# Kernel optimization log

Hardware: AMD Instinct MI355X
Metric: run time of the kernel (lower is better)

The kernel has to match this reference:

```python
import jax, jax.numpy as jnp
import numpy as np

VOCAB, EMB, HID, NCLASS = 32000, 256, 512, 16
SEQ, BATCH = 512, 128


def setup_inputs() -> dict:
    key = jax.random.key(0)
    ks = jax.random.split(key, 8)
    s = 1.0 / np.sqrt(HID)
    return {
        "x": jax.random.randint(ks[0], (SEQ, BATCH), 0, VOCAB, dtype=jnp.int32),
        "emb": jax.random.normal(ks[1], (VOCAB, EMB), dtype=jnp.float32),
        "W_ih": jax.random.uniform(ks[2], (HID, EMB), jnp.float32, -s, s),
        "W_hh": jax.random.uniform(ks[3], (HID, HID), jnp.float32, -s, s),
        "b_ih": jax.random.uniform(ks[4], (HID,), jnp.float32, -s, s),
        "b_hh": jax.random.uniform(ks[5], (HID,), jnp.float32, -s, s),
        "W_fc": jax.random.uniform(ks[6], (NCLASS, HID), jnp.float32, -s, s),
        "b_fc": jax.random.uniform(ks[7], (NCLASS,), jnp.float32, -s, s),
    }


def reference(x, emb, W_ih, W_hh, b_ih, b_hh, W_fc, b_fc):
    # embedding lookup: [S, B] -> [S, B, E]
    xe = emb[x]
    # precompute input projections for all timesteps: [S, B, H]
    xproj = jnp.einsum("sbe,he->sbh", xe, W_ih) + b_ih + b_hh

    def step(h, xp_t):
        h_new = jnp.tanh(xp_t + h @ W_hh.T)
        return h_new, None

    h0 = jnp.zeros((xe.shape[1], W_hh.shape[0]), dtype=xe.dtype)
    h_last, _ = jax.lax.scan(step, h0, xproj)
    # final linear on last timestep's hidden state: [B, NCLASS]
    return h_last @ W_fc.T + b_fc
```

## Files before the change

### kernel.cpp

```cpp
#include <hip/hip_runtime.h>
#include <hip/hip_bf16.h>

#define SEQ   512
#define BATCH 128
#define EMBD  256
#define HIDD  512
#define NCLS  16
#define VOCAB 32000

typedef unsigned long long u64;
typedef __attribute__((ext_vector_type(8))) short  short8;
typedef __attribute__((ext_vector_type(4))) float  f32x4;
typedef __attribute__((ext_vector_type(4))) int    i32x4;

__device__ __forceinline__ float bfu(unsigned short u) {
    return __uint_as_float(((unsigned int)u) << 16);
}
__device__ __forceinline__ unsigned short f2bf(float f) {
    __hip_bfloat16 h = __float2bfloat16(f);
    return *reinterpret_cast<unsigned short*>(&h);
}
__device__ __forceinline__ float rcp_fast(float x) {
    float r;
    asm("v_rcp_f32 %0, %1" : "=v"(r) : "v"(x));
    return r;
}
__device__ __forceinline__ unsigned q127b(float x) {
    const float e = __expf(x + x);
    const float r = rcp_fast(e + 1.f);
    const float f = fmaf(r, -254.f, 12583039.f);
    return __float_as_uint(f);
}
__device__ __forceinline__ unsigned pack4(unsigned a, unsigned b,
                                          unsigned c, unsigned d) {
    const unsigned lo = __builtin_amdgcn_perm(b, a, 0x0400u);
    const unsigned hi = __builtin_amdgcn_perm(d, c, 0x0400u);
    return __builtin_amdgcn_perm(hi, lo, 0x05040100u);
}
__device__ __forceinline__ void ep_store(unsigned short* p, float v) { *p = f2bf(v); }

__device__ __forceinline__ void lds_barrier() {
    __builtin_amdgcn_sched_barrier(0);
    asm volatile("s_waitcnt lgkmcnt(0)" ::: "memory");
    __builtin_amdgcn_s_barrier();
    __builtin_amdgcn_sched_barrier(0);
}

__global__ void init_scl(float* __restrict__ scl) {
    if (threadIdx.x == 0) reinterpret_cast<unsigned*>(scl)[2] = 0u;
}

__global__ __launch_bounds__(256) void absmax_whh2(const float* __restrict__ W,
                                                   float* __restrict__ scl) {
    __shared__ float red[256];
    float m = 0.f;
    for (int i = blockIdx.x * 256 + threadIdx.x; i < (HIDD * HIDD) / 4; i += 64 * 256) {
        const float4 v = reinterpret_cast<const float4*>(W)[i];
        m = fmaxf(m, fmaxf(fmaxf(fabsf(v.x), fabsf(v.y)),
                           fmaxf(fabsf(v.z), fabsf(v.w))));
    }
    red[threadIdx.x] = m;
    __syncthreads();
    for (int s = 128; s > 0; s >>= 1) {
        if (threadIdx.x < s) red[threadIdx.x] = fmaxf(red[threadIdx.x], red[threadIdx.x + s]);
        __syncthreads();
    }
    if (threadIdx.x == 0)
        atomicMax(reinterpret_cast<unsigned*>(scl) + 2, __float_as_uint(red[0]));
}

__global__ void quant_whh2(const float* __restrict__ W, float* __restrict__ scl,
                           signed char* __restrict__ Wq) {
    const int i = blockIdx.x * 256 + threadIdx.x;
    const float am  = __uint_as_float(reinterpret_cast<unsigned*>(scl)[2]);
    const float inv = 127.f / am;
    Wq[i] = (signed char)(int)rintf(W[i] * inv);
    if (i == 0) { scl[0] = am; scl[1] = am / 16129.f; }
}

__global__ void cvt_wih(const float* __restrict__ W, unsigned short* __restrict__ Wb) {
    const int i = blockIdx.x * 256 + threadIdx.x;
    Wb[i] = f2bf(W[i]);
}

__global__ __launch_bounds__(256) void ep_gemm3(
    const float* __restrict__ emb, const unsigned short* __restrict__ Wih_b,
    const float* __restrict__ b_ih, const float* __restrict__ b_hh,
    unsigned short* __restrict__ EP) {
    const int w = threadIdx.x >> 6, l = threadIdx.x & 63;
    const int n = l & 15, lk = l >> 4;
    const int mtile = blockIdx.x * 4 + w;
    const int arow  = mtile * 16 + n;

    short8 areg[8];
    #pragma unroll
    for (int kk = 0; kk < 8; ++kk) {
        const int k0 = kk * 32 + lk * 8;
        const float4 a0 = *reinterpret_cast<const float4*>(emb + arow * EMBD + k0);
        const float4 a1 = *reinterpret_cast<const float4*>(emb + arow * EMBD + k0 + 4);
        short8 t;
        t[0]=(short)f2bf(a0.x); t[1]=(short)f2bf(a0.y); t[2]=(short)f2bf(a0.z); t[3]=(short)f2bf(a0.w);
        t[4]=(short)f2bf(a1.x); t[5]=(short)f2bf(a1.y); t[6]=(short)f2bf(a1.z); t[7]=(short)f2bf(a1.w);
        areg[kk] = t;
    }

    for (int nt = 0; nt < 32; ++nt) {
        const int col  = nt * 16 + n;
        const float bias = b_ih[col] + b_hh[col];
        f32x4 accA = {0.f,0.f,0.f,0.f}, accB = {0.f,0.f,0.f,0.f};
        #pragma unroll
        for (int kk = 0; kk < 8; ++kk) {
            const short8 bb = *reinterpret_cast<const short8*>(
                Wih_b + (size_t)col * EMBD + kk * 32 + lk * 8);
            if (kk & 1) accB = __builtin_amdgcn_mfma_f32_16x16x32_bf16(areg[kk], bb, accB, 0, 0, 0);
            else        accA = __builtin_amdgcn_mfma_f32_16x16x32_bf16(areg[kk], bb, accA, 0, 0, 0);
        }
        const f32x4 ac = accA + accB;
        #pragma unroll
        for (int r = 0; r < 4; ++r)
            ep_store(EP + (size_t)(mtile * 16 + lk * 4 + r) * HIDD + col, ac[r] + bias);
    }
}

__global__ __launch_bounds__(512, 2) void rnn11(
    const int*            __restrict__ x,
    const signed char*    __restrict__ Wq,
    const float*          __restrict__ scl,
    const unsigned short* __restrict__ EP,
    const float*          __restrict__ W_fc,
    const float*          __restrict__ b_fc,
    float*                __restrict__ out) {

    __shared__ __align__(16) char hq[2 * 16 * 512];

    const int tid = threadIdx.x;
    const int w   = tid >> 6, l = tid & 63;
    const int n   = l & 15,  lk = l >> 4;
    const int b0  = blockIdx.x * 16;
    const int jw  = w * 64;
    const float fs = scl[1];

    int rdA[8];
    #pragma unroll
    for (int kf = 0; kf < 8; ++kf) {
        const int g = kf * 4 + lk;
        rdA[kf] = n * 512 + ((g ^ n) << 4);
    }
    int wrA[4];
    #pragma unroll
    for (int tau = 0; tau < 4; ++tau) {
        const int j0 = jw + tau * 16 + lk * 4;
        wrA[tau] = n * 512 + (((j0 >> 4) ^ n) << 4) + (j0 & 15);
    }

    const unsigned short* const epb = EP + jw + lk * 4;

    i32x4 af[4][8];
    #pragma unroll
    for (int tau = 0; tau < 4; ++tau)
        #pragma unroll
        for (int kf = 0; kf < 8; ++kf)
            af[tau][kf] = *reinterpret_cast<const i32x4*>(
                Wq + (size_t)(jw + tau * 16 + n) * HIDD + kf * 64 + lk * 16);

    {
        const int tok0 = x[b0 + n];
        #pragma unroll
        for (int tau = 0; tau < 4; ++tau) {
            const ushort4 v = *reinterpret_cast<const ushort4*>(
                epb + (size_t)tok0 * HIDD + tau * 16);
            *reinterpret_cast<unsigned*>(hq + 8192 + wrA[tau]) =
                pack4(q127b(bfu(v.x)), q127b(bfu(v.y)),
                      q127b(bfu(v.z)), q127b(bfu(v.w)));
        }
    }

    ushort4 pcA[4], pcB[4];
    int tokA, tokB;
    {
        const int tok1 = x[BATCH + b0 + n];
        #pragma unroll
        for (int tau = 0; tau < 4; ++tau)
            pcA[tau] = *reinterpret_cast<const ushort4*>(
                epb + (size_t)tok1 * HIDD + tau * 16);
    }
    tokB = x[2 * BATCH + b0 + n];
    __syncthreads();

#define FIN(tau, acc, PC, WO)                                                 \
    {                                                                         \
        const unsigned q0 = q127b(fmaf((float)acc[0], fs, bfu(PC[tau].x)));   \
        const unsigned q1 = q127b(fmaf((float)acc[1], fs, bfu(PC[tau].y)));   \
        const unsigned q2 = q127b(fmaf((float)acc[2], fs, bfu(PC[tau].z)));   \
        const unsigned q3 = q127b(fmaf((float)acc[3], fs, bfu(PC[tau].w)));   \
        *reinterpret_cast<unsigned*>(hq + (WO) + wrA[tau]) = pack4(q0, q1, q2, q3); \
    }
#define STEP(ro, wo, PC, PN, TOKIN, TOKOUT, TNEXT)                            \
    {                                                                         \
        _Pragma("unroll")                                                     \
        for (int tau = 0; tau < 4; ++tau)                                     \
            PN[tau] = *reinterpret_cast<const ushort4*>(                      \
                epb + (size_t)(TOKIN) * HIDD + tau * 16);                     \
        const int tn_ = (TNEXT) > 511 ? 511 : (TNEXT);                        \
        TOKOUT = x[tn_ * BATCH + b0 + n];                                     \
        i32x4 B[8];                                                           \
        _Pragma("unroll")                                                     \
        for (int kf = 0; kf < 8; ++kf)                                        \
            B[kf] = *reinterpret_cast<const i32x4*>(hq + (ro) + rdA[kf]);     \
        i32x4 a0 = {0,0,0,0}, a1 = {0,0,0,0}, a2 = {0,0,0,0}, a3 = {0,0,0,0}; \
        _Pragma("unroll")                                                     \
        for (int kf = 0; kf < 8; ++kf) {                                      \
            a0 = __builtin_amdgcn_mfma_i32_16x16x64_i8(af[0][kf], B[kf], a0, 0, 0, 0); \
            a1 = __builtin_amdgcn_mfma_i32_16x16x64_i8(af[1][kf], B[kf], a1, 0, 0, 0); \
            a2 = __builtin_amdgcn_mfma_i32_16x16x64_i8(af[2][kf], B[kf], a2, 0, 0, 0); \
            a3 = __builtin_amdgcn_mfma_i32_16x16x64_i8(af[3][kf], B[kf], a3, 0, 0, 0); \
        }                                                                     \
        FIN(0, a0, PC, wo) FIN(1, a1, PC, wo)                                 \
        FIN(2, a2, PC, wo) FIN(3, a3, PC, wo)                                 \
        lds_barrier();                                                        \
    }

    for (int tp = 0; tp < 256; ++tp) {
        const int t = 2 * tp + 1;
        STEP(8192, 0, pcA, pcB, tokB, tokA, t + 2)
        if (t == 511) break;
        STEP(0, 8192, pcB, pcA, tokA, tokB, t + 3)
    }
#undef STEP
#undef FIN

    if (tid < 256) {
        const int n2 = tid >> 4, c = tid & 15;
        float dot = 0.f;
        for (int g = 0; g < 32; ++g) {
            const char* p = hq + n2 * 512 + ((g ^ n2) << 4);
            const float* wf = W_fc + c * HIDD + g * 16;
            #pragma unroll
            for (int i = 0; i < 16; ++i)
                dot += (float)((signed char)p[i]) * wf[i];
        }
        out[(b0 + n2) * NCLS + c] = dot * (1.f / 127.f) + b_fc[c];
    }
}

__global__ void cvt_kernel(const float* __restrict__ W_ih,
                           const float* __restrict__ W_hh,
                           const float* __restrict__ b_ih,
                           const float* __restrict__ b_hh,
                           unsigned short* __restrict__ Wpk,
                           unsigned short* __restrict__ Wipk,
                           float* __restrict__ bias) {
    const int NW = HIDD * HIDD;
    const int NI = HIDD * EMBD;
    int gid = blockIdx.x * blockDim.x + threadIdx.x;
    if (gid < NW) {
        int j = gid >> 9, k = gid & (HIDD - 1);
        Wpk[((k >> 2) * HIDD + j) * 4 + (k & 3)] = f2bf(W_hh[gid]);
    } else if (gid < NW + NI) {
        int g2 = gid - NW, j = g2 >> 8, e = g2 & (EMBD - 1);
        Wipk[((e >> 2) * HIDD + j) * 4 + (e & 3)] = f2bf(W_ih[g2]);
    } else if (gid < NW + NI + HIDD) {
        int j = gid - NW - NI;
        bias[j] = b_ih[j] + b_hh[j];
    }
}

__global__ __launch_bounds__(512) void rnn_kernel(
    const int* __restrict__ x, const float* __restrict__ emb,
    const unsigned short* __restrict__ Wpk, const unsigned short* __restrict__ Wipk,
    const float* __restrict__ bias, const float* __restrict__ W_fc,
    const float* __restrict__ b_fc, float* __restrict__ out) {
    __shared__ __align__(16) float hL[HIDD];
    __shared__ __align__(16) float xe[EMBD];
    __shared__ float red[512];
    const int tid = threadIdx.x, b = blockIdx.x, j = tid;
    hL[j] = 0.0f;
    const float bj = bias[j];
    const ushort4* Wp4 = reinterpret_cast<const ushort4*>(Wpk);
    const ushort4* Wi4 = reinterpret_cast<const ushort4*>(Wipk);
    for (int t = 0; t < SEQ; ++t) {
        const int tok = x[t * BATCH + b];
        if (tid < EMBD) xe[tid] = emb[tok * EMBD + tid];
        __syncthreads();
        float a0 = bj, a1 = 0.0f;
        #pragma unroll 8
        for (int e4 = 0; e4 < EMBD / 4; ++e4) {
            const float4 xv = *reinterpret_cast<const float4*>(&xe[e4 * 4]);
            const ushort4 ww = Wi4[e4 * HIDD + j];
            a0 += xv.x * bfu(ww.x) + xv.y * bfu(ww.y);
            a1 += xv.z * bfu(ww.z) + xv.w * bfu(ww.w);
        }
        #pragma unroll 8
        for (int k4 = 0; k4 < HIDD / 4; ++k4) {
            const float4 hvv = *reinterpret_cast<const float4*>(&hL[k4 * 4]);
            const ushort4 ww = Wp4[k4 * HIDD + j];
            a0 += hvv.x * bfu(ww.x) + hvv.y * bfu(ww.y);
            a1 += hvv.z * bfu(ww.z) + hvv.w * bfu(ww.w);
        }
        __syncthreads();
        hL[j] = tanhf(a0 + a1);
    }
    __syncthreads();
    {
        const int c = tid >> 5, ks = tid & 31;
        float p = 0.0f;
        #pragma unroll
        for (int jj = 0; jj < HIDD / 32; ++jj) {
            const int jd = ks * (HIDD / 32) + jj;
            p += hL[jd] * W_fc[c * HIDD + jd];
        }
        red[tid] = p;
        __syncthreads();
        if (tid < NCLS) {
            float ss = b_fc[tid];
            #pragma unroll
            for (int i = 0; i < 32; ++i) ss += red[tid * 32 + i];
            out[b * NCLS + tid] = ss;
        }
    }
}

extern "C" void kernel_launch(void* const* d_in, const int* in_sizes, int n_in,
                              void* d_out, int out_size, void* d_ws, size_t ws_size,
                              hipStream_t stream) {
    const int*   x    = (const int*)  d_in[0];
    const float* emb  = (const float*)d_in[1];
    const float* W_ih = (const float*)d_in[2];
    const float* W_hh = (const float*)d_in[3];
    const float* b_ih = (const float*)d_in[4];
    const float* b_hh = (const float*)d_in[5];
    const float* W_fc = (const float*)d_in[6];
    const float* b_fc = (const float*)d_in[7];
    float* out = (float*)d_out;

    const size_t QW_B  = (size_t)HIDD * HIDD;
    const size_t SCL_B = 16;
    const size_t WIH_B = (size_t)HIDD * EMBD * 2;
    const size_t EPN   = (size_t)VOCAB * HIDD;
    const size_t HEAD  = QW_B + SCL_B + WIH_B;

    if (ws_size >= HEAD + EPN * 2) {
        signed char*    Wq    = (signed char*)d_ws;
        float*          scl   = (float*)((char*)d_ws + QW_B);
        unsigned short* Wih_b = (unsigned short*)((char*)d_ws + QW_B + SCL_B);
        unsigned short* EP    = (unsigned short*)((char*)d_ws + HEAD);
        init_scl<<<1, 64, 0, stream>>>(scl);
        absmax_whh2<<<64, 256, 0, stream>>>(W_hh, scl);
        quant_whh2<<<(HIDD * HIDD) / 256, 256, 0, stream>>>(W_hh, scl, Wq);
        cvt_wih<<<(HIDD * EMBD) / 256, 256, 0, stream>>>(W_ih, Wih_b);
        ep_gemm3<<<VOCAB / 64, 256, 0, stream>>>(emb, Wih_b, b_ih, b_hh, EP);
        rnn11<<<8, 512, 0, stream>>>(x, Wq, scl, EP, W_fc, b_fc, out);
    } else {
        unsigned short* Wpk  = (unsigned short*)d_ws;
        unsigned short* Wipk = Wpk + HIDD * HIDD;
        float*          bias = (float*)(Wipk + HIDD * EMBD);
        const int total = HIDD * HIDD + HIDD * EMBD + HIDD;
        cvt_kernel<<<(total + 255) / 256, 256, 0, stream>>>(W_ih, W_hh, b_ih, b_hh, Wpk, Wipk, bias);
        rnn_kernel<<<BATCH, 512, 0, stream>>>(x, emb, Wpk, Wipk, bias, W_fc, b_fc, out);
    }
}
```

Measured before the change: 786.2 us.

## Split hidden columns across 16 waves per block in int8 RNN recurrence

Doubles the block size to 1024 threads so each wave computes 32 hidden outputs instead of 64 per timestep, halving the per-wave MFMA chain on the serial recurrence. The h-vector fragment loads are split into two halves of four to lower register pressure. In exchange, every wave still reads the full hidden state from LDS, doubling LDS read traffic, and the per-step barrier now synchronises twice as many waves.

Result: slower. 930.8 us (+18.4%).

```diff
diff --git a/kernel.cpp b/kernel.cpp
--- a/kernel.cpp
+++ b/kernel.cpp
@@ -122,7 +122,7 @@
     }
 }
 
-__global__ __launch_bounds__(512, 2) void rnn11(
+__global__ __launch_bounds__(1024, 4) void rnn12(
     const int*            __restrict__ x,
     const signed char*    __restrict__ Wq,
     const float*          __restrict__ scl,
@@ -137,7 +137,7 @@
     const int w   = tid >> 6, l = tid & 63;
     const int n   = l & 15,  lk = l >> 4;
     const int b0  = blockIdx.x * 16;
-    const int jw  = w * 64;
+    const int jw  = w * 32;
     const float fs = scl[1];
 
     int rdA[8];
@@ -146,18 +146,18 @@
         const int g = kf * 4 + lk;
         rdA[kf] = n * 512 + ((g ^ n) << 4);
     }
-    int wrA[4];
+    int wrA[2];
     #pragma unroll
-    for (int tau = 0; tau < 4; ++tau) {
+    for (int tau = 0; tau < 2; ++tau) {
         const int j0 = jw + tau * 16 + lk * 4;
         wrA[tau] = n * 512 + (((j0 >> 4) ^ n) << 4) + (j0 & 15);
     }
 
     const unsigned short* const epb = EP + jw + lk * 4;
 
-    i32x4 af[4][8];
+    i32x4 af[2][8];
     #pragma unroll
-    for (int tau = 0; tau < 4; ++tau)
+    for (int tau = 0; tau < 2; ++tau)
         #pragma unroll
         for (int kf = 0; kf < 8; ++kf)
             af[tau][kf] = *reinterpret_cast<const i32x4*>(
@@ -166,7 +166,7 @@
     {
         const int tok0 = x[b0 + n];
         #pragma unroll
-        for (int tau = 0; tau < 4; ++tau) {
+        for (int tau = 0; tau < 2; ++tau) {
             const ushort4 v = *reinterpret_cast<const ushort4*>(
                 epb + (size_t)tok0 * HIDD + tau * 16);
             *reinterpret_cast<unsigned*>(hq + 8192 + wrA[tau]) =
@@ -175,12 +175,12 @@
         }
     }
 
-    ushort4 pcA[4], pcB[4];
+    ushort4 pcA[2], pcB[2];
     int tokA, tokB;
     {
         const int tok1 = x[BATCH + b0 + n];
         #pragma unroll
-        for (int tau = 0; tau < 4; ++tau)
+        for (int tau = 0; tau < 2; ++tau)
             pcA[tau] = *reinterpret_cast<const ushort4*>(
                 epb + (size_t)tok1 * HIDD + tau * 16);
     }
@@ -197,26 +197,36 @@
     }
 #define STEP(ro, wo, PC, PN, TOKIN, TOKOUT, TNEXT)                            \
     {                                                                         \
-        _Pragma("unroll")                                                     \
-        for (int tau = 0; tau < 4; ++tau)                                     \
-            PN[tau] = *reinterpret_cast<const ushort4*>(                      \
-                epb + (size_t)(TOKIN) * HIDD + tau * 16);                     \
+        PN[0] = *reinterpret_cast<const ushort4*>(                            \
+            epb + (size_t)(TOKIN) * HIDD);                                    \
+        PN[1] = *reinterpret_cast<const ushort4*>(                            \
+            epb + (size_t)(TOKIN) * HIDD + 16);                               \
         const int tn_ = (TNEXT) > 511 ? 511 : (TNEXT);                        \
         TOKOUT = x[tn_ * BATCH + b0 + n];                                     \
-        i32x4 B[8];                                                           \
-        _Pragma("unroll")                                                     \
-        for (int kf = 0; kf < 8; ++kf)                                        \
-            B[kf] = *reinterpret_cast<const i32x4*>(hq + (ro) + rdA[kf]);     \
-        i32x4 a0 = {0,0,0,0}, a1 = {0,0,0,0}, a2 = {0,0,0,0}, a3 = {0,0,0,0}; \
-        _Pragma("unroll")                                                     \
-        for (int kf = 0; kf < 8; ++kf) {                                      \
-            a0 = __builtin_amdgcn_mfma_i32_16x16x64_i8(af[0][kf], B[kf], a0, 0, 0, 0); \
-            a1 = __builtin_amdgcn_mfma_i32_16x16x64_i8(af[1][kf], B[kf], a1, 0, 0, 0); \
-            a2 = __builtin_amdgcn_mfma_i32_16x16x64_i8(af[2][kf], B[kf], a2, 0, 0, 0); \
-            a3 = __builtin_amdgcn_mfma_i32_16x16x64_i8(af[3][kf], B[kf], a3, 0, 0, 0); \
+        i32x4 a0 = {0,0,0,0}, a1 = {0,0,0,0};                                 \
+        {                                                                     \
+            i32x4 Bt[4];                                                      \
+            _Pragma("unroll")                                                 \
+            for (int kf = 0; kf < 4; ++kf)                                    \
+                Bt[kf] = *reinterpret_cast<const i32x4*>(hq + (ro) + rdA[kf]);\
+            _Pragma("unroll")                                                 \
+            for (int kf = 0; kf < 4; ++kf) {                                  \
+                a0 = __builtin_amdgcn_mfma_i32_16x16x64_i8(af[0][kf], Bt[kf], a0, 0, 0, 0); \
+                a1 = __builtin_amdgcn_mfma_i32_16x16x64_i8(af[1][kf], Bt[kf], a1, 0, 0, 0); \
+            }                                                                 \
+        }                                                                     \
+        {                                                                     \
+            i32x4 Bt[4];                                                      \
+            _Pragma("unroll")                                                 \
+            for (int kf = 0; kf < 4; ++kf)                                    \
+                Bt[kf] = *reinterpret_cast<const i32x4*>(hq + (ro) + rdA[kf + 4]);\
+            _Pragma("unroll")                                                 \
+            for (int kf = 0; kf < 4; ++kf) {                                  \
+                a0 = __builtin_amdgcn_mfma_i32_16x16x64_i8(af[0][kf + 4], Bt[kf], a0, 0, 0, 0); \
+                a1 = __builtin_amdgcn_mfma_i32_16x16x64_i8(af[1][kf + 4], Bt[kf], a1, 0, 0, 0); \
+            }                                                                 \
         }                                                                     \
         FIN(0, a0, PC, wo) FIN(1, a1, PC, wo)                                 \
-        FIN(2, a2, PC, wo) FIN(3, a3, PC, wo)                                 \
         lds_barrier();                                                        \
     }
 
@@ -349,7 +359,7 @@
         quant_whh2<<<(HIDD * HIDD) / 256, 256, 0, stream>>>(W_hh, scl, Wq);
         cvt_wih<<<(HIDD * EMBD) / 256, 256, 0, stream>>>(W_ih, Wih_b);
         ep_gemm3<<<VOCAB / 64, 256, 0, stream>>>(emb, Wih_b, b_ih, b_hh, EP);
-        rnn11<<<8, 512, 0, stream>>>(x, Wq, scl, EP, W_fc, b_fc, out);
+        rnn12<<<8, 1024, 0, stream>>>(x, Wq, scl, EP, W_fc, b_fc, out);
     } else {
         unsigned short* Wpk  = (unsigned short*)d_ws;
         unsigned short* Wipk = Wpk + HIDD * HIDD;
```
